# Kernel tuning notes

Hardware: AMD Instinct MI355X
Metric: run time of the kernel (lower is better)

## Reference

```python
import jax, jax.numpy as jnp
import numpy as np

B, N, D, C = 32, 8192, 256, 1000  # batch, nodes, dim (dim_original == dim_attention), num_class


def setup_inputs() -> dict:
    key = jax.random.key(0)
    ks = jax.random.split(key, 6)
    s = 1.0 / np.sqrt(D)
    return {
        "atom": jax.random.normal(ks[0], (B, N, D), dtype=jnp.float32),
        "obj": jax.random.normal(ks[1], (B, D), dtype=jnp.float32),
        "W": jax.random.uniform(ks[2], (D, D), jnp.float32, -s, s),        # nn.Linear(D, D, bias=False).weight
        "A": jax.random.uniform(ks[3], (1, 2 * D), jnp.float32, -1.0 / np.sqrt(2 * D), 1.0 / np.sqrt(2 * D)),  # nn.Linear(2D, 1, bias=False).weight
        "CW": jax.random.uniform(ks[4], (C, 2 * D), jnp.float32, -1.0 / np.sqrt(2 * D), 1.0 / np.sqrt(2 * D)),  # classifier weight
        "CB": jax.random.uniform(ks[5], (C,), jnp.float32, -1.0 / np.sqrt(2 * D), 1.0 / np.sqrt(2 * D)),        # classifier bias
    }


def reference(atom, obj, W, A, CW, CB):
    # a1 = w(atom): [B, N, D]; o1 = w(obj): [B, D]
    a1 = jnp.einsum("bnd,kd->bnk", atom, W)
    o1 = obj @ W.T
    # att = Linear_a(cat(a1, broadcast(o1)))  == a1 @ A1 + o1 @ A2 (no concat materialized)
    A1, A2 = A[0, :D], A[0, D:]
    att = a1 @ A1 + (o1 @ A2)[:, None]          # [B, N] attention scores (no softmax)
    # message_a2o = att_weights.bmm(a1).squeeze(): [B, D]
    msg = jnp.einsum("bn,bnd->bd", att, a1)
    # inte == 'concat': classifier(cat(o1, msg))
    preds = jnp.concatenate([o1, msg], axis=-1) @ CW.T + CB  # [B, C]
    return preds
```

## Files before the change

### kernel.cpp

```cpp
#include <hip/hip_runtime.h>

#define DD 256
#define BB 32
#define NN 8192
#define CC 1000
#define SUBS 32

typedef float f4 __attribute__((ext_vector_type(4)));

__device__ __forceinline__ f4 ntload(const float* p) {
    return __builtin_nontemporal_load((const f4*)p);
}

template <int CTRL>
__device__ __forceinline__ float dpp_ror_add(float s) {
    int r = __builtin_amdgcn_update_dpp(0, __float_as_int(s), CTRL, 0xF, 0xF, true);
    return s + __int_as_float(r);
}
__device__ __forceinline__ float rowsum16(float s) {
    s = dpp_ror_add<0x121>(s);
    s = dpp_ror_add<0x122>(s);
    s = dpp_ror_add<0x124>(s);
    s = dpp_ror_add<0x128>(s);
    return s;
}

__global__ __launch_bounds__(256) void k_prep(const float* __restrict__ W,
                                              const float* __restrict__ A,
                                              const float* __restrict__ obj,
                                              float* __restrict__ v1,
                                              float* __restrict__ c) {
    int b = blockIdx.x, t = threadIdx.x;
    int q  = t >> 6;
    int cs = (t & 63) * 4;
    __shared__ float s1[4][DD], s2[4][DD];
    __shared__ float sc[4];
    f4 a1 = {0.f, 0.f, 0.f, 0.f}, a2 = a1;
#pragma unroll 8
    for (int k = q; k < DD; k += 4) {
        f4 w = *(const f4*)(W + (size_t)k * DD + cs);
        a1 += A[k] * w;
        a2 += A[DD + k] * w;
    }
    *(f4*)&s1[q][cs] = a1;
    *(f4*)&s2[q][cs] = a2;
    __syncthreads();
    float vv1 = s1[0][t] + s1[1][t] + s1[2][t] + s1[3][t];
    float vv2 = s2[0][t] + s2[1][t] + s2[2][t] + s2[3][t];
    if (b == 0) v1[t] = vv1;
    float p = vv2 * obj[(size_t)b * DD + t];
    p = rowsum16(p);
    p += __shfl_xor(p, 16, 64);
    p += __shfl_xor(p, 32, 64);
    if ((t & 63) == 0) sc[t >> 6] = p;
    __syncthreads();
    if (t == 0) c[b] = sc[0] + sc[1] + sc[2] + sc[3];
}

__global__ __launch_bounds__(256, 4) void k_main(const float* __restrict__ atom,
                                                 const float* __restrict__ v1,
                                                 const float* __restrict__ c,
                                                 float* __restrict__ partials) {
    int blk  = blockIdx.x;
    int b    = blk >> 5;
    int sub  = blk & 31;
    int tid  = threadIdx.x;
    int wave = tid >> 6, lane = tid & 63;
    int grp  = lane >> 4, gl = lane & 15;

    __shared__ float sv1[DD];
    __shared__ float tsh[4][DD];
    sv1[tid] = v1[tid];
    __syncthreads();
    float4 w0 = *(const float4*)&sv1[gl * 4];
    float4 w1 = *(const float4*)&sv1[gl * 4 + 64];
    float4 w2 = *(const float4*)&sv1[gl * 4 + 128];
    float4 w3 = *(const float4*)&sv1[gl * 4 + 192];
    float  cb = c[b];

    const float* p = atom + ((size_t)b * NN + (size_t)sub * 256 + wave * 64 + grp) * DD
                   + gl * 4;

    f4 A0 = {0.f, 0.f, 0.f, 0.f}, A1 = A0, A2 = A0, A3 = A0;

#pragma unroll 4
    for (int g = 0; g < 16; ++g) {
        f4 x0 = ntload(p);
        f4 x1 = ntload(p + 64);
        f4 x2 = ntload(p + 128);
        f4 x3 = ntload(p + 192);
        p += 4 * DD;
        float dot = x0.x * w0.x + x0.y * w0.y + x0.z * w0.z + x0.w * w0.w
                  + x1.x * w1.x + x1.y * w1.y + x1.z * w1.z + x1.w * w1.w
                  + x2.x * w2.x + x2.y * w2.y + x2.z * w2.z + x2.w * w2.w
                  + x3.x * w3.x + x3.y * w3.y + x3.z * w3.z + x3.w * w3.w;
        float att = rowsum16(dot) + cb;
        A0 += att * x0;
        A1 += att * x1;
        A2 += att * x2;
        A3 += att * x3;
    }

#define XRED(v)                              \
    v.x += __shfl_xor(v.x, 16, 64); v.x += __shfl_xor(v.x, 32, 64); \
    v.y += __shfl_xor(v.y, 16, 64); v.y += __shfl_xor(v.y, 32, 64); \
    v.z += __shfl_xor(v.z, 16, 64); v.z += __shfl_xor(v.z, 32, 64); \
    v.w += __shfl_xor(v.w, 16, 64); v.w += __shfl_xor(v.w, 32, 64);
    XRED(A0) XRED(A1) XRED(A2) XRED(A3)
#undef XRED

    if (grp == 0) {
        *(f4*)&tsh[wave][gl * 4]       = A0;
        *(f4*)&tsh[wave][gl * 4 + 64]  = A1;
        *(f4*)&tsh[wave][gl * 4 + 128] = A2;
        *(f4*)&tsh[wave][gl * 4 + 192] = A3;
    }
    __syncthreads();
    partials[(size_t)blk * DD + tid] =
        tsh[0][tid] + tsh[1][tid] + tsh[2][tid] + tsh[3][tid];
}

__global__ __launch_bounds__(256) void k_mid(const float* __restrict__ partials,
                                             const float* __restrict__ W,
                                             const float* __restrict__ obj,
                                             float* __restrict__ x) {
    int b = blockIdx.x >> 4, q = blockIdx.x & 15;
    int t = threadIdx.x;
    __shared__ float tt[DD];
    __shared__ float so[DD];

    float s = 0.f;
#pragma unroll 8
    for (int i = 0; i < SUBS; ++i) s += partials[((size_t)(b * SUBS + i)) * DD + t];
    tt[t] = s;
    so[t] = obj[(size_t)b * DD + t];
    __syncthreads();

    int kk = t >> 4, cs = t & 15;
    int k  = q * 16 + kk;
    const float4* wr = (const float4*)(W + (size_t)k * DD + cs * 16);
    float p = 0.f, po = 0.f;
#pragma unroll
    for (int ii = 0; ii < 4; ++ii) {
        int i = (ii + cs) & 3;
        float4 a  = wr[i];
        float4 xx = *(const float4*)&tt[cs * 16 + i * 4];
        float4 oo = *(const float4*)&so[cs * 16 + i * 4];
        p  += a.x * xx.x + a.y * xx.y + a.z * xx.z + a.w * xx.w;
        po += a.x * oo.x + a.y * oo.y + a.z * oo.z + a.w * oo.w;
    }
    p  = rowsum16(p);
    po = rowsum16(po);
    if (cs == 0) {
        x[b * 2 * DD + DD + k] = p;
        x[b * 2 * DD + k]      = po;
    }
}

__global__ __launch_bounds__(256) void k_class(const float* __restrict__ x,
                                               const float* __restrict__ CW,
                                               const float* __restrict__ CB,
                                               float* __restrict__ out) {
    int bg = blockIdx.x / 63, ch = blockIdx.x % 63;
    int t = threadIdx.x;
    __shared__ float xs[8][2 * DD];

    {
        const f4* src = (const f4*)(x + (size_t)bg * 8 * 2 * DD);
        f4* dst = (f4*)&xs[0][0];
#pragma unroll
        for (int i = 0; i < 4; ++i) dst[t + 256 * i] = src[t + 256 * i];
    }
    __syncthreads();

    int cl = t >> 4, seg = t & 15;
    int j = ch * 16 + cl;
    if (j < CC) {
        const f4* cw = (const f4*)(CW + (size_t)j * 2 * DD + seg * 32);
        float p[8];
#pragma unroll
        for (int bb = 0; bb < 8; ++bb) p[bb] = 0.f;
#pragma unroll
        for (int ii = 0; ii < 8; ++ii) {
            int i = (ii + seg) & 7;
            f4 a = cw[i];
#pragma unroll
            for (int bb = 0; bb < 8; ++bb) {
                f4 v = *(const f4*)&xs[bb][seg * 32 + i * 4];
                p[bb] += a.x * v.x + a.y * v.y + a.z * v.z + a.w * v.w;
            }
        }
#pragma unroll
        for (int bb = 0; bb < 8; ++bb) p[bb] = rowsum16(p[bb]);
        if (seg == 0) {
            float cb = CB[j];
            int b0 = bg * 8;
#pragma unroll
            for (int bb = 0; bb < 8; ++bb)
                out[(size_t)(b0 + bb) * CC + j] = p[bb] + cb;
        }
    }
}

extern "C" void kernel_launch(void* const* d_in, const int* in_sizes, int n_in,
                              void* d_out, int out_size, void* d_ws, size_t ws_size,
                              hipStream_t stream) {
    const float* atom = (const float*)d_in[0];
    const float* obj  = (const float*)d_in[1];
    const float* W    = (const float*)d_in[2];
    const float* A    = (const float*)d_in[3];
    const float* CW   = (const float*)d_in[4];
    const float* CB   = (const float*)d_in[5];
    float* out = (float*)d_out;

    float* ws = (float*)d_ws;
    float* v1       = ws;
    float* c        = ws + 256;
    float* x        = ws + 512;
    float* partials = x + (size_t)BB * 2 * DD;

    hipLaunchKernelGGL(k_prep,  dim3(BB),        dim3(256), 0, stream, W, A, obj, v1, c);
    hipLaunchKernelGGL(k_main,  dim3(BB * SUBS), dim3(256), 0, stream, atom, v1, c, partials);
    hipLaunchKernelGGL(k_mid,   dim3(BB * 16),   dim3(256), 0, stream, partials, W, obj, x);
    hipLaunchKernelGGL(k_class, dim3(4 * 63),    dim3(256), 0, stream, x, CW, CB, out);
}
```

Measured before the change: 68.48 us.

## Fuse mid-stage W projection into main kernel via per-batch atomic counter

Removes the separate k_mid launch. After writing its partial sum, each k_main block increments a per-batch atomic counter, which k_prep now zeroes. The last 16 blocks to arrive per batch spin until all 32 partials are written, then each computes one 16-row slice of the W projection for msg and obj. Nontemporal loads of atom are also replaced with plain loads. This saves a launch and its gap, but the spin-wait relies on all blocks of a batch being co-resident or already finished, which adds a risk of stalls or deadlock.

```diff
diff --git a/kernel.cpp b/kernel.cpp
--- a/kernel.cpp
+++ b/kernel.cpp
@@ -7,10 +7,6 @@
 #define SUBS 32
 
 typedef float f4 __attribute__((ext_vector_type(4)));
-
-__device__ __forceinline__ f4 ntload(const float* p) {
-    return __builtin_nontemporal_load((const f4*)p);
-}
 
 template <int CTRL>
 __device__ __forceinline__ float dpp_ror_add(float s) {
@@ -29,8 +25,10 @@
                                               const float* __restrict__ A,
                                               const float* __restrict__ obj,
                                               float* __restrict__ v1,
-                                              float* __restrict__ c) {
+                                              float* __restrict__ c,
+                                              int* __restrict__ counter) {
     int b = blockIdx.x, t = threadIdx.x;
+    if (t == 0) counter[b] = 0;
     int q  = t >> 6;
     int cs = (t & 63) * 4;
     __shared__ float s1[4][DD], s2[4][DD];
@@ -60,7 +58,11 @@
 __global__ __launch_bounds__(256, 4) void k_main(const float* __restrict__ atom,
                                                  const float* __restrict__ v1,
                                                  const float* __restrict__ c,
-                                                 float* __restrict__ partials) {
+                                                 const float* __restrict__ obj,
+                                                 const float* __restrict__ W,
+                                                 float* __restrict__ partials,
+                                                 float* __restrict__ x,
+                                                 int* __restrict__ counter) {
     int blk  = blockIdx.x;
     int b    = blk >> 5;
     int sub  = blk & 31;
@@ -70,6 +72,7 @@
 
     __shared__ float sv1[DD];
     __shared__ float tsh[4][DD];
+    __shared__ int rank_sh;
     sv1[tid] = v1[tid];
     __syncthreads();
     float4 w0 = *(const float4*)&sv1[gl * 4];
@@ -85,10 +88,10 @@
 
 #pragma unroll 4
     for (int g = 0; g < 16; ++g) {
-        f4 x0 = ntload(p);
-        f4 x1 = ntload(p + 64);
-        f4 x2 = ntload(p + 128);
-        f4 x3 = ntload(p + 192);
+        f4 x0 = *(const f4*)(p);
+        f4 x1 = *(const f4*)(p + 64);
+        f4 x2 = *(const f4*)(p + 128);
+        f4 x3 = *(const f4*)(p + 192);
         p += 4 * DD;
         float dot = x0.x * w0.x + x0.y * w0.y + x0.z * w0.z + x0.w * w0.w
                   + x1.x * w1.x + x1.y * w1.y + x1.z * w1.z + x1.w * w1.w
@@ -118,41 +121,46 @@
     __syncthreads();
     partials[(size_t)blk * DD + tid] =
         tsh[0][tid] + tsh[1][tid] + tsh[2][tid] + tsh[3][tid];
-}
-
-__global__ __launch_bounds__(256) void k_mid(const float* __restrict__ partials,
-                                             const float* __restrict__ W,
-                                             const float* __restrict__ obj,
-                                             float* __restrict__ x) {
-    int b = blockIdx.x >> 4, q = blockIdx.x & 15;
-    int t = threadIdx.x;
-    __shared__ float tt[DD];
-    __shared__ float so[DD];
+
+    __threadfence();
+    __syncthreads();
+    if (tid == 0) rank_sh = atomicAdd(&counter[b], 1);
+    __syncthreads();
+    int rank = rank_sh;
+    if (rank < SUBS - 16) return;
+    int q = rank - 16;
+
+    if (tid == 0) {
+        while (atomicAdd(&counter[b], 0) < SUBS) {}
+    }
+    __syncthreads();
+    __threadfence();
 
     float s = 0.f;
 #pragma unroll 8
-    for (int i = 0; i < SUBS; ++i) s += partials[((size_t)(b * SUBS + i)) * DD + t];
-    tt[t] = s;
-    so[t] = obj[(size_t)b * DD + t];
-    __syncthreads();
-
-    int kk = t >> 4, cs = t & 15;
+    for (int i = 0; i < SUBS; ++i)
+        s += partials[((size_t)(b * SUBS + i)) * DD + tid];
+    sv1[tid]    = s;
+    tsh[0][tid] = obj[(size_t)b * DD + tid];
+    __syncthreads();
+
+    int kk = tid >> 4, cs = tid & 15;
     int k  = q * 16 + kk;
     const float4* wr = (const float4*)(W + (size_t)k * DD + cs * 16);
-    float p = 0.f, po = 0.f;
+    float pm = 0.f, po = 0.f;
 #pragma unroll
     for (int ii = 0; ii < 4; ++ii) {
         int i = (ii + cs) & 3;
         float4 a  = wr[i];
-        float4 xx = *(const float4*)&tt[cs * 16 + i * 4];
-        float4 oo = *(const float4*)&so[cs * 16 + i * 4];
-        p  += a.x * xx.x + a.y * xx.y + a.z * xx.z + a.w * xx.w;
+        float4 xx = *(const float4*)&sv1[cs * 16 + i * 4];
+        float4 oo = *(const float4*)&tsh[0][cs * 16 + i * 4];
+        pm += a.x * xx.x + a.y * xx.y + a.z * xx.z + a.w * xx.w;
         po += a.x * oo.x + a.y * oo.y + a.z * oo.z + a.w * oo.w;
     }
-    p  = rowsum16(p);
+    pm = rowsum16(pm);
     po = rowsum16(po);
     if (cs == 0) {
-        x[b * 2 * DD + DD + k] = p;
+        x[b * 2 * DD + DD + k] = pm;
         x[b * 2 * DD + k]      = po;
     }
 }
@@ -218,9 +226,10 @@
     float* c        = ws + 256;
     float* x        = ws + 512;
     float* partials = x + (size_t)BB * 2 * DD;
-
-    hipLaunchKernelGGL(k_prep,  dim3(BB),        dim3(256), 0, stream, W, A, obj, v1, c);
-    hipLaunchKernelGGL(k_main,  dim3(BB * SUBS), dim3(256), 0, stream, atom, v1, c, partials);
-    hipLaunchKernelGGL(k_mid,   dim3(BB * 16),   dim3(256), 0, stream, partials, W, obj, x);
+    int*   counter  = (int*)(partials + (size_t)BB * SUBS * DD);
+
+    hipLaunchKernelGGL(k_prep,  dim3(BB),        dim3(256), 0, stream, W, A, obj, v1, c, counter);
+    hipLaunchKernelGGL(k_main,  dim3(BB * SUBS), dim3(256), 0, stream,
+                       atom, v1, c, obj, W, partials, x, counter);
     hipLaunchKernelGGL(k_class, dim3(4 * 63),    dim3(256), 0, stream, x, CW, CB, out);
 }
```

After: 247.5 us. 3.62x slower.
